# Optimization experiments

Measured on AMD Instinct MI355X. Metric: run time of the kernel, lower is better.

## Reference

```python
import jax, jax.numpy as jnp
import numpy as np

BN_EPS = 1e-5
MIN_DIST = 1e-10

def _three_nn(xyz_up, xyz_down):
    # Pairwise squared distances (B, N, M) via expansion: ||a-b||^2 = |a|^2 + |b|^2 - 2 a.b
    up_sq = jnp.sum(xyz_up * xyz_up, axis=-1, keepdims=True)        # (B, N, 1)
    down_sq = jnp.sum(xyz_down * xyz_down, axis=-1)[:, None, :]      # (B, 1, M)
    cross = jnp.einsum('bnd,bmd->bnm', xyz_up, xyz_down)             # (B, N, M)
    d2 = up_sq + down_sq - 2.0 * cross
    neg_vals, idx = jax.lax.top_k(-d2, 3)                            # 3 smallest dists
    return -neg_vals, idx                                            # (B,N,3), (B,N,3)

def _three_interpolate(features_down, idx, weight):
    # features_down: (B, C, M); idx, weight: (B, N, 3) -> (B, C, N)
    f = jnp.transpose(features_down, (0, 2, 1))                      # (B, M, C)
    gathered = jax.vmap(lambda fm, im: fm[im])(f, idx)               # (B, N, 3, C)
    interp = jnp.einsum('bnkc,bnk->bcn', gathered, weight)           # (B, C, N)
    return interp

def _conv_bn_relu(x, W, gamma, beta):
    # x: (B, C_in, N); W: (C_out, C_in) 1x1 conv, no bias
    y = jnp.einsum('oc,bcn->bon', W, x)
    mean = jnp.mean(y, axis=(0, 2), keepdims=True)
    var = jnp.mean((y - mean) ** 2, axis=(0, 2), keepdims=True)      # biased var (torch BN)
    y = (y - mean) * jax.lax.rsqrt(var + BN_EPS)
    y = y * gamma[None, :, None] + beta[None, :, None]
    return jax.nn.relu(y)

def setup_inputs() -> dict:
    key = jax.random.key(0)
    ks = jax.random.split(key, 8)
    B, N, M = 8, 8192, 2048
    C_down, C_skip = 256, 128
    C_in = C_down + C_skip
    xyz_up = jax.random.normal(ks[0], (B, N, 3), dtype=jnp.float32)
    xyz_down = jax.random.normal(ks[1], (B, M, 3), dtype=jnp.float32)
    features_up = jax.random.normal(ks[2], (B, C_skip, N), dtype=jnp.float32)
    features_down = jax.random.normal(ks[3], (B, C_down, M), dtype=jnp.float32)
    W1 = jax.random.normal(ks[4], (256, C_in), dtype=jnp.float32) * (1.0 / np.sqrt(C_in))
    W2 = jax.random.normal(ks[5], (256, 256), dtype=jnp.float32) * (1.0 / np.sqrt(256))
    g1 = jnp.ones((256,), jnp.float32); b1 = jnp.zeros((256,), jnp.float32)
    g2 = jnp.ones((256,), jnp.float32); b2 = jnp.zeros((256,), jnp.float32)
    return {"xyz_up": xyz_up, "xyz_down": xyz_down, "features_up": features_up,
            "features_down": features_down, "W1": W1, "g1": g1, "b1": b1,
            "W2": W2, "g2": g2, "b2": b2}

def reference(xyz_up, xyz_down, features_up, features_down, W1, g1, b1, W2, g2, b2):
    dist_sq, idx = _three_nn(xyz_up, xyz_down)
    dist_sq = jnp.maximum(dist_sq, MIN_DIST)
    weight = 1.0 / dist_sq
    weight = weight / jnp.sum(weight, axis=-1, keepdims=True)
    interpolated = _three_interpolate(features_down, idx, weight)    # (B, C_down, N)
    combined = jnp.concatenate([interpolated, features_up], axis=1)  # (B, C_in, N)
    h = _conv_bn_relu(combined, W1, g1, b1)
    out = _conv_bn_relu(h, W2, g2, b2)
    return out
```

## Files before the change

kernel.cpp:

```cpp
#include <hip/hip_runtime.h>
#include <hip/hip_bf16.h>

#define NB 8
#define NQ 8192
#define MP 2048
#define CDW 256
#define CSK 128
#define CIN 384
#define COUT 256

typedef __bf16 bf16_t;
typedef bf16_t bf16x8 __attribute__((ext_vector_type(8)));
typedef float f32x4 __attribute__((ext_vector_type(4)));

static __device__ __forceinline__ float bf2f(unsigned short u){
  union { unsigned int ui; float f; } v; v.ui = ((unsigned int)u) << 16; return v.f;
}
static __device__ __forceinline__ unsigned short f2bf(float f){
  union { float f; unsigned int u; } v; v.f = f;
  unsigned int u = v.u;
  return (unsigned short)((u + 0x7FFFu + ((u >> 16) & 1u)) >> 16);
}

__global__ void k_cvt_w(const float* __restrict__ W1, const float* __restrict__ W2,
                        unsigned short* __restrict__ W1b, unsigned short* __restrict__ W2b){
  int i = blockIdx.x * 256 + threadIdx.x;
  if (i < COUT*CIN) W1b[i] = f2bf(W1[i]);
  if (i < COUT*COUT) W2b[i] = f2bf(W2[i]);
}

__global__ __launch_bounds__(256) void k_z(const unsigned short* __restrict__ W1b,
    const float* __restrict__ fd, unsigned short* __restrict__ Z){
  __shared__ unsigned short Bl[64][264];
  int b = blockIdx.y, m0 = blockIdx.x << 6;
  int t = threadIdx.x;
  {
    int m = t & 63, cs0 = t >> 6;
    for (int it = 0; it < 64; ++it){
      int c = cs0 + (it << 2);
      Bl[m][c] = f2bf(fd[((size_t)b*CDW + c)*MP + m0 + m]);
    }
  }
  __syncthreads();
  int l = t & 63, wv = t >> 6;
  int lr = l & 15, lg = l >> 4;
  int ob = wv << 6;
  f32x4 acc[4][4];
  #pragma unroll
  for (int i = 0; i < 4; ++i)
    #pragma unroll
    for (int j = 0; j < 4; ++j)
      acc[i][j] = (f32x4){0.f, 0.f, 0.f, 0.f};
  #pragma unroll 1
  for (int kt = 0; kt < 8; ++kt){
    int k0 = (kt << 5) + (lg << 3);
    bf16x8 af[4], bv[4];
    #pragma unroll
    for (int of = 0; of < 4; ++of)
      af[of] = *(const bf16x8*)(W1b + (size_t)(ob + (of<<4) + lr)*CIN + k0);
    #pragma unroll
    for (int nf = 0; nf < 4; ++nf)
      bv[nf] = *(const bf16x8*)&Bl[(nf<<4) + lr][k0];
    #pragma unroll
    for (int of = 0; of < 4; ++of)
      #pragma unroll
      for (int nf = 0; nf < 4; ++nf)
        acc[of][nf] = __builtin_amdgcn_mfma_f32_16x16x32_bf16(af[of], bv[nf], acc[of][nf], 0, 0, 0);
  }
  #pragma unroll
  for (int of = 0; of < 4; ++of){
    int o = ob + (of<<4) + (lg<<2);
    #pragma unroll
    for (int nf = 0; nf < 4; ++nf){
      int m = m0 + (nf<<4) + lr;
      ushort4 pk;
      pk.x = f2bf(acc[of][nf][0]);
      pk.y = f2bf(acc[of][nf][1]);
      pk.z = f2bf(acc[of][nf][2]);
      pk.w = f2bf(acc[of][nf][3]);
      *(ushort4*)(Z + (((size_t)b*MP + m) << 8) + o) = pk;
    }
  }
}

#define CHUNKS 4
#define MC (MP/CHUNKS)
__global__ __launch_bounds__(256, 2) void k_nn_part(const float* __restrict__ xu, const float* __restrict__ xd,
                                                    float* __restrict__ pd, int* __restrict__ pi){
  int b = blockIdx.z, ch = blockIdx.y, nt = blockIdx.x;
  int t = threadIdx.x;
  __shared__ float4 pts[MC];
  const float* xdb = xd + ((size_t)b*MP + (size_t)ch*MC)*3;
  for (int p = t; p < MC; p += 256){
    float x = xdb[p*3+0], y = xdb[p*3+1], z = xdb[p*3+2];
    pts[p] = make_float4(x, y, z, -0.5f*(x*x + y*y + z*z));
  }
  __syncthreads();
  int n = nt*256 + t;
  const float* q = xu + ((size_t)b*NQ + n)*3;
  float qx = q[0], qy = q[1], qz = q[2];
  float qs = qx*qx + qy*qy + qz*qz;
  float s0 = -3.4e38f, s1 = -3.4e38f, s2 = -3.4e38f;
  int i0 = 0, i1 = 0, i2 = 0;
  #pragma unroll 8
  for (int m = 0; m < MC; ++m){
    float4 p = pts[m];
    float s = fmaf(qz, p.z, fmaf(qy, p.y, fmaf(qx, p.x, p.w)));
    bool c0 = s > s0, c1 = s > s1, c2 = s > s2;
    s2 = c1 ? s1 : (c2 ? s : s2);
    i2 = c1 ? i1 : (c2 ? m : i2);
    s1 = c0 ? s0 : (c1 ? s : s1);
    i1 = c0 ? i0 : (c1 ? m : i1);
    s0 = c0 ? s : s0;
    i0 = c0 ? m : i0;
  }
  int gb = ch*MC;
  size_t base = (((size_t)b*CHUNKS + ch)*NQ + n)*3;
  pd[base+0] = qs - 2.f*s0; pd[base+1] = qs - 2.f*s1; pd[base+2] = qs - 2.f*s2;
  pi[base+0] = gb + i0; pi[base+1] = gb + i1; pi[base+2] = gb + i2;
}

__global__ void k_nn_merge(const float* __restrict__ pd, const int* __restrict__ pi,
                           int* __restrict__ idx3, float* __restrict__ w3){
  int gid = blockIdx.x * 256 + threadIdx.x;
  int b = gid >> 13, n = gid & (NQ-1);
  float d0 = 3.4e38f, d1 = 3.4e38f, d2 = 3.4e38f;
  int i0 = 0, i1 = 0, i2 = 0;
  for (int ch = 0; ch < CHUNKS; ++ch){
    size_t base = (((size_t)b*CHUNKS + ch)*NQ + n)*3;
    #pragma unroll
    for (int k = 0; k < 3; ++k){
      float d = pd[base + k]; int gm = pi[base + k];
      bool c0 = d < d0, c1 = d < d1, c2 = d < d2;
      d2 = c1 ? d1 : (c2 ? d : d2);  i2 = c1 ? i1 : (c2 ? gm : i2);
      d1 = c0 ? d0 : (c1 ? d : d1);  i1 = c0 ? i0 : (c1 ? gm : i1);
      d0 = c0 ? d : d0;              i0 = c0 ? gm : i0;
    }
  }
  float w0 = 1.f / fmaxf(d0, 1e-10f);
  float w1 = 1.f / fmaxf(d1, 1e-10f);
  float w2 = 1.f / fmaxf(d2, 1e-10f);
  float s = w0 + w1 + w2;
  idx3[gid*3+0] = i0; idx3[gid*3+1] = i1; idx3[gid*3+2] = i2;
  w3[gid*3+0] = w0/s; w3[gid*3+1] = w1/s; w3[gid*3+2] = w2/s;
}

__global__ __launch_bounds__(256) void k_fused1(const unsigned short* __restrict__ W1b,
    const float* __restrict__ fu, const int* __restrict__ idx3, const float* __restrict__ w3,
    const unsigned short* __restrict__ Z,
    unsigned short* __restrict__ Y1, float* __restrict__ Sp, float* __restrict__ SSp){
  __shared__ unsigned short Xl[64][136];
  int tile = blockIdx.x;
  int b = tile >> 7;
  int n0 = (tile & 127) << 6;
  int t = threadIdx.x;
  {
    int n = t & 63, cs0 = t >> 6;
    for (int it = 0; it < 32; ++it){
      int cs = cs0 + (it << 2);
      Xl[n][cs] = f2bf(fu[((size_t)b*CSK + cs)*NQ + n0 + n]);
    }
  }
  __syncthreads();
  int l = t & 63, wv = t >> 6;
  int lr = l & 15, lg = l >> 4;
  int ob = wv << 6;
  f32x4 acc[4][4];
  #pragma unroll
  for (int i = 0; i < 4; ++i)
    #pragma unroll
    for (int j = 0; j < 4; ++j)
      acc[i][j] = (f32x4){0.f, 0.f, 0.f, 0.f};
  #pragma unroll 1
  for (int kt = 0; kt < 4; ++kt){
    int k0 = (kt << 5) + (lg << 3);
    bf16x8 af[4], bv[4];
    #pragma unroll
    for (int of = 0; of < 4; ++of)
      af[of] = *(const bf16x8*)(W1b + (size_t)(ob + (of<<4) + lr)*CIN + 256 + k0);
    #pragma unroll
    for (int nf = 0; nf < 4; ++nf)
      bv[nf] = *(const bf16x8*)&Xl[(nf<<4) + lr][k0];
    #pragma unroll
    for (int of = 0; of < 4; ++of)
      #pragma unroll
      for (int nf = 0; nf < 4; ++nf)
        acc[of][nf] = __builtin_amdgcn_mfma_f32_16x16x32_bf16(af[of], bv[nf], acc[of][nf], 0, 0, 0);
  }
  const unsigned short* Zb = Z + (((size_t)b*MP) << 8);
  #pragma unroll
  for (int nf = 0; nf < 4; ++nf){
    int nn = n0 + (nf<<4) + lr;
    int q = ((b << 13) + nn) * 3;
    int j0 = idx3[q], j1 = idx3[q+1], j2 = idx3[q+2];
    float w0 = w3[q], w1 = w3[q+1], w2 = w3[q+2];
    const unsigned short* z0p = Zb + ((size_t)j0 << 8);
    const unsigned short* z1p = Zb + ((size_t)j1 << 8);
    const unsigned short* z2p = Zb + ((size_t)j2 << 8);
    #pragma unroll
    for (int of = 0; of < 4; ++of){
      int o = ob + (of<<4) + (lg<<2);
      ushort4 z0 = *(const ushort4*)(z0p + o);
      ushort4 z1 = *(const ushort4*)(z1p + o);
      ushort4 z2 = *(const ushort4*)(z2p + o);
      acc[of][nf][0] += w0*bf2f(z0.x) + w1*bf2f(z1.x) + w2*bf2f(z2.x);
      acc[of][nf][1] += w0*bf2f(z0.y) + w1*bf2f(z1.y) + w2*bf2f(z2.y);
      acc[of][nf][2] += w0*bf2f(z0.z) + w1*bf2f(z1.z) + w2*bf2f(z2.z);
      acc[of][nf][3] += w0*bf2f(z0.w) + w1*bf2f(z1.w) + w2*bf2f(z2.w);
    }
  }
  #pragma unroll
  for (int of = 0; of < 4; ++of){
    int o = ob + (of<<4) + (lg<<2);
    #pragma unroll
    for (int nf = 0; nf < 4; ++nf){
      int n = n0 + (nf<<4) + lr;
      size_t pos = ((size_t)b << 13) + n;
      ushort4 pk;
      pk.x = f2bf(acc[of][nf][0]);
      pk.y = f2bf(acc[of][nf][1]);
      pk.z = f2bf(acc[of][nf][2]);
      pk.w = f2bf(acc[of][nf][3]);
      *(ushort4*)(Y1 + pos*COUT + o) = pk;
    }
  }
  #pragma unroll
  for (int of = 0; of < 4; ++of){
    #pragma unroll
    for (int r = 0; r < 4; ++r){
      float sv = acc[of][0][r] + acc[of][1][r] + acc[of][2][r] + acc[of][3][r];
      float sq = acc[of][0][r]*acc[of][0][r] + acc[of][1][r]*acc[of][1][r]
               + acc[of][2][r]*acc[of][2][r] + acc[of][3][r]*acc[of][3][r];
      #pragma unroll
      for (int off = 1; off < 16; off <<= 1){
        sv += __shfl_xor(sv, off);
        sq += __shfl_xor(sq, off);
      }
      if (lr == 0){
        int o = ob + (of<<4) + (lg<<2) + r;
        Sp[(size_t)tile*256 + o] = sv;
        SSp[(size_t)tile*256 + o] = sq;
      }
    }
  }
}

__global__ __launch_bounds__(256) void k_reduce(const float* __restrict__ Sp, const float* __restrict__ SSp,
                                                float* __restrict__ Sr, float* __restrict__ SSr){
  int t = threadIdx.x;
  int w = blockIdx.x * 4 + (t >> 6);
  int lane = t & 63;
  const float* src = (w < 256) ? Sp : SSp;
  int o = w & 255;
  float s = 0.f;
  #pragma unroll
  for (int j = 0; j < 16; ++j)
    s += src[(size_t)(lane + (j << 6))*256 + o];
  #pragma unroll
  for (int off = 1; off < 64; off <<= 1) s += __shfl_xor(s, off);
  if (lane == 0){
    if (w < 256) Sr[o] = s; else SSr[o] = s;
  }
}

__global__ void k_finalize(const float* __restrict__ S, const float* __restrict__ SS,
                           const float* __restrict__ g, const float* __restrict__ be,
                           float* __restrict__ scale, float* __restrict__ shift){
  int o = threadIdx.x;
  const float cnt = 65536.f;
  float mean = S[o] / cnt;
  float var = SS[o] / cnt - mean*mean;
  float inv = rsqrtf(var + 1e-5f);
  float sc = g[o] * inv;
  scale[o] = sc;
  shift[o] = be[o] - mean * sc;
}

__global__ __launch_bounds__(256) void k_gemm2(const unsigned short* __restrict__ W2b,
    const unsigned short* __restrict__ Y1, const float* __restrict__ scale1,
    const float* __restrict__ shift1, unsigned short* __restrict__ Y2,
    float* __restrict__ Sp, float* __restrict__ SSp){
  __shared__ unsigned short buf[256*68];
  int tile = blockIdx.x;
  int b = tile >> 7;
  int n0 = (tile & 127) << 6;
  int t = threadIdx.x;
  {
    int nn0 = t >> 6;
    int cb = (t & 63) << 2;
    float scl[4], shl[4];
    #pragma unroll
    for (int j = 0; j < 4; ++j){ scl[j] = scale1[cb+j]; shl[j] = shift1[cb+j]; }
    for (int it = 0; it < 16; ++it){
      int nn = nn0 + (it << 2);
      size_t pos = ((size_t)b << 13) + n0 + nn;
      ushort4 a = *(const ushort4*)(Y1 + pos*COUT + cb);
      ushort4 r;
      r.x = f2bf(fmaxf(bf2f(a.x)*scl[0] + shl[0], 0.f));
      r.y = f2bf(fmaxf(bf2f(a.y)*scl[1] + shl[1], 0.f));
      r.z = f2bf(fmaxf(bf2f(a.z)*scl[2] + shl[2], 0.f));
      r.w = f2bf(fmaxf(bf2f(a.w)*scl[3] + shl[3], 0.f));
      *(ushort4*)&buf[nn*264 + cb] = r;
    }
  }
  __syncthreads();
  int l = t & 63, wv = t >> 6;
  int lr = l & 15, lg = l >> 4;
  int ob = wv << 6;
  f32x4 acc[4][4];
  #pragma unroll
  for (int i = 0; i < 4; ++i)
    #pragma unroll
    for (int j = 0; j < 4; ++j)
      acc[i][j] = (f32x4){0.f, 0.f, 0.f, 0.f};
  #pragma unroll 1
  for (int kt = 0; kt < 8; ++kt){
    int k0 = (kt << 5) + (lg << 3);
    bf16x8 af[4], bv[4];
    #pragma unroll
    for (int of = 0; of < 4; ++of)
      af[of] = *(const bf16x8*)(W2b + (size_t)(ob + (of<<4) + lr)*COUT + k0);
    #pragma unroll
    for (int nf = 0; nf < 4; ++nf)
      bv[nf] = *(const bf16x8*)&buf[((nf<<4) + lr)*264 + k0];
    #pragma unroll
    for (int of = 0; of < 4; ++of)
      #pragma unroll
      for (int nf = 0; nf < 4; ++nf)
        acc[of][nf] = __builtin_amdgcn_mfma_f32_16x16x32_bf16(af[of], bv[nf], acc[of][nf], 0, 0, 0);
  }
  #pragma unroll
  for (int of = 0; of < 4; ++of){
    #pragma unroll
    for (int r = 0; r < 4; ++r){
      float sv = acc[of][0][r] + acc[of][1][r] + acc[of][2][r] + acc[of][3][r];
      float sq = acc[of][0][r]*acc[of][0][r] + acc[of][1][r]*acc[of][1][r]
               + acc[of][2][r]*acc[of][2][r] + acc[of][3][r]*acc[of][3][r];
      #pragma unroll
      for (int off = 1; off < 16; off <<= 1){
        sv += __shfl_xor(sv, off);
        sq += __shfl_xor(sq, off);
      }
      if (lr == 0){
        int o = ob + (of<<4) + (lg<<2) + r;
        Sp[(size_t)tile*256 + o] = sv;
        SSp[(size_t)tile*256 + o] = sq;
      }
    }
  }
  __syncthreads();
  #pragma unroll
  for (int of = 0; of < 4; ++of){
    int o = ob + (of<<4) + (lg<<2);
    #pragma unroll
    for (int nf = 0; nf < 4; ++nf){
      int n = (nf<<4) + lr;
      #pragma unroll
      for (int r = 0; r < 4; ++r)
        buf[(o + r)*68 + n] = f2bf(acc[of][nf][r]);
    }
  }
  __syncthreads();
  {
    int nx = (t & 31) << 1;
    int og = t >> 5;
    for (int it = 0; it < 32; ++it){
      int o = og + (it << 3);
      unsigned int v = (unsigned int)buf[o*68 + nx] | ((unsigned int)buf[o*68 + nx + 1] << 16);
      *(unsigned int*)(Y2 + (((size_t)b*COUT + o) << 13) + n0 + nx) = v;
    }
  }
}

__global__ void k_out(const unsigned short* __restrict__ Y2,
                      const float* __restrict__ scale2, const float* __restrict__ shift2,
                      float* __restrict__ out){
  size_t i = (size_t)blockIdx.x * 256 + threadIdx.x;
  size_t e = i << 2;
  int o = (int)((e >> 13) & 255);
  ushort4 v = *(const ushort4*)(Y2 + e);
  float sc = scale2[o], sh = shift2[o];
  float4 r;
  r.x = fmaxf(bf2f(v.x)*sc + sh, 0.f);
  r.y = fmaxf(bf2f(v.y)*sc + sh, 0.f);
  r.z = fmaxf(bf2f(v.z)*sc + sh, 0.f);
  r.w = fmaxf(bf2f(v.w)*sc + sh, 0.f);
  *(float4*)(out + e) = r;
}

extern "C" void kernel_launch(void* const* d_in, const int* in_sizes, int n_in,
                              void* d_out, int out_size, void* d_ws, size_t ws_size,
                              hipStream_t stream) {
  (void)in_sizes; (void)n_in; (void)out_size; (void)ws_size;
  const float* xu = (const float*)d_in[0];
  const float* xd = (const float*)d_in[1];
  const float* fu = (const float*)d_in[2];
  const float* fd = (const float*)d_in[3];
  const float* W1 = (const float*)d_in[4];
  const float* g1 = (const float*)d_in[5];
  const float* b1 = (const float*)d_in[6];
  const float* W2 = (const float*)d_in[7];
  const float* g2 = (const float*)d_in[8];
  const float* b2 = (const float*)d_in[9];
  float* out = (float*)d_out;

  char* w = (char*)d_ws;
  size_t off = 0;
  unsigned short* Z   = (unsigned short*)(w + off); off += (size_t)NB*MP*256*2;
  unsigned short* W1b = (unsigned short*)(w + off); off += (size_t)COUT*CIN*2;
  unsigned short* W2b = (unsigned short*)(w + off); off += (size_t)COUT*COUT*2;
  float* pd  = (float*)(w + off); off += (size_t)NB*CHUNKS*NQ*3*4;
  int*   pi  = (int*)(w + off);   off += (size_t)NB*CHUNKS*NQ*3*4;
  int*   idx3= (int*)(w + off);   off += (size_t)NB*NQ*3*4;
  float* w3  = (float*)(w + off); off += (size_t)NB*NQ*3*4;
  unsigned short* Y1 = (unsigned short*)(w + off); off += (size_t)NB*NQ*COUT*2;
  unsigned short* Y2 = (unsigned short*)(w + off); off += (size_t)NB*NQ*COUT*2;
  float* Sp1  = (float*)(w + off); off += (size_t)1024*256*4;
  float* SSp1 = (float*)(w + off); off += (size_t)1024*256*4;
  float* Sp2  = (float*)(w + off); off += (size_t)1024*256*4;
  float* SSp2 = (float*)(w + off); off += (size_t)1024*256*4;
  float* Sr1  = (float*)(w + off); off += 256*4;
  float* SSr1 = (float*)(w + off); off += 256*4;
  float* Sr2  = (float*)(w + off); off += 256*4;
  float* SSr2 = (float*)(w + off); off += 256*4;
  float* scale1 = (float*)(w + off); off += 256*4;
  float* shift1 = (float*)(w + off); off += 256*4;
  float* scale2 = (float*)(w + off); off += 256*4;
  float* shift2 = (float*)(w + off); off += 256*4;

  k_cvt_w<<<dim3(384), dim3(256), 0, stream>>>(W1, W2, W1b, W2b);
  k_z<<<dim3(32, 8), dim3(256), 0, stream>>>(W1b, fd, Z);
  k_nn_part<<<dim3(32, 4, 8), dim3(256), 0, stream>>>(xu, xd, pd, pi);
  k_nn_merge<<<dim3(256), dim3(256), 0, stream>>>(pd, pi, idx3, w3);
  k_fused1<<<dim3(1024), dim3(256), 0, stream>>>(W1b, fu, idx3, w3, Z, Y1, Sp1, SSp1);
  k_reduce<<<dim3(128), dim3(256), 0, stream>>>(Sp1, SSp1, Sr1, SSr1);
  k_finalize<<<dim3(1), dim3(256), 0, stream>>>(Sr1, SSr1, g1, b1, scale1, shift1);
  k_gemm2<<<dim3(1024), dim3(256), 0, stream>>>(W2b, Y1, scale1, shift1, Y2, Sp2, SSp2);
  k_reduce<<<dim3(128), dim3(256), 0, stream>>>(Sp2, SSp2, Sr2, SSr2);
  k_finalize<<<dim3(1), dim3(256), 0, stream>>>(Sr2, SSr2, g2, b2, scale2, shift2);
  k_out<<<dim3(16384), dim3(256), 0, stream>>>(Y2, scale2, shift2, out);
}
```

Before: 189.8 us.

## Process two queries per thread with inline-asm top-3 in NN search

The nearest-neighbour partial kernel now has each thread track two query points, so every shared-memory point load is reused for two distance evaluations. The top-3 insertion is written as hand-scheduled v_fma/v_cmp/v_cndmask inline assembly, interleaved across the two queries for more instruction-level parallelism. To keep the block count the same, the point set is split into 8 chunks instead of 4. In exchange, the merge kernel reads twice as many partial candidates, and the pd/pi workspace must be sized for 8 chunks.

```diff
diff --git a/kernel.cpp b/kernel.cpp
--- a/kernel.cpp
+++ b/kernel.cpp
@@ -83,41 +83,93 @@
   }
 }
 
-#define CHUNKS 4
+#define CHUNKS 8
 #define MC (MP/CHUNKS)
+
+#define NN_STEP2(P)                                                          \
+  asm("v_fma_f32 %[sa], %[qxa], %[px], %[pw]\n\t"                            \
+      "v_fma_f32 %[sb], %[qxb], %[px], %[pw]\n\t"                            \
+      "v_fma_f32 %[sa], %[qya], %[py], %[sa]\n\t"                            \
+      "v_fma_f32 %[sb], %[qyb], %[py], %[sb]\n\t"                            \
+      "v_fma_f32 %[sa], %[qza], %[pz], %[sa]\n\t"                            \
+      "v_fma_f32 %[sb], %[qzb], %[pz], %[sb]\n\t"                            \
+      "v_cmp_gt_f32 %[m1a], %[sa], %[s1a]\n\t"                               \
+      "v_cmp_gt_f32 %[m1b], %[sb], %[s1b]\n\t"                               \
+      "v_cmp_gt_f32 %[m2a], %[sa], %[s2a]\n\t"                               \
+      "v_cmp_gt_f32 %[m2b], %[sb], %[s2b]\n\t"                               \
+      "v_cndmask_b32 %[s2a], %[s2a], %[sa], %[m2a]\n\t"                      \
+      "v_cndmask_b32 %[s2b], %[s2b], %[sb], %[m2b]\n\t"                      \
+      "v_cndmask_b32 %[i2a], %[i2a], %[mi], %[m2a]\n\t"                      \
+      "v_cndmask_b32 %[i2b], %[i2b], %[mi], %[m2b]\n\t"                      \
+      "v_cndmask_b32 %[s2a], %[s2a], %[s1a], %[m1a]\n\t"                     \
+      "v_cndmask_b32 %[s2b], %[s2b], %[s1b], %[m1b]\n\t"                     \
+      "v_cndmask_b32 %[i2a], %[i2a], %[i1a], %[m1a]\n\t"                     \
+      "v_cndmask_b32 %[i2b], %[i2b], %[i1b], %[m1b]\n\t"                     \
+      "v_cmp_gt_f32 %[m2a], %[sa], %[s0a]\n\t"                               \
+      "v_cmp_gt_f32 %[m2b], %[sb], %[s0b]\n\t"                               \
+      "v_cndmask_b32 %[s1a], %[s1a], %[sa], %[m1a]\n\t"                      \
+      "v_cndmask_b32 %[s1b], %[s1b], %[sb], %[m1b]\n\t"                      \
+      "v_cndmask_b32 %[i1a], %[i1a], %[mi], %[m1a]\n\t"                      \
+      "v_cndmask_b32 %[i1b], %[i1b], %[mi], %[m1b]\n\t"                      \
+      "v_cndmask_b32 %[s1a], %[s1a], %[s0a], %[m2a]\n\t"                     \
+      "v_cndmask_b32 %[s1b], %[s1b], %[s0b], %[m2b]\n\t"                     \
+      "v_cndmask_b32 %[i1a], %[i1a], %[i0a], %[m2a]\n\t"                     \
+      "v_cndmask_b32 %[i1b], %[i1b], %[i0b], %[m2b]\n\t"                     \
+      "v_cndmask_b32 %[s0a], %[s0a], %[sa], %[m2a]\n\t"                      \
+      "v_cndmask_b32 %[s0b], %[s0b], %[sb], %[m2b]\n\t"                      \
+      "v_cndmask_b32 %[i0a], %[i0a], %[mi], %[m2a]\n\t"                      \
+      "v_cndmask_b32 %[i0b], %[i0b], %[mi], %[m2b]\n\t"                      \
+      "v_add_u32 %[mi], 1, %[mi]\n\t"                                        \
+      : [sa]"=&v"(sva), [sb]"=&v"(svb),                                      \
+        [m1a]"=&s"(mk1a), [m2a]"=&s"(mk2a), [m1b]"=&s"(mk1b), [m2b]"=&s"(mk2b),\
+        [s0a]"+v"(s0a), [s1a]"+v"(s1a), [s2a]"+v"(s2a),                      \
+        [i0a]"+v"(i0a), [i1a]"+v"(i1a), [i2a]"+v"(i2a),                      \
+        [s0b]"+v"(s0b), [s1b]"+v"(s1b), [s2b]"+v"(s2b),                      \
+        [i0b]"+v"(i0b), [i1b]"+v"(i1b), [i2b]"+v"(i2b), [mi]"+v"(mi)         \
+      : [qxa]"v"(qxa), [qya]"v"(qya), [qza]"v"(qza),                         \
+        [qxb]"v"(qxb), [qyb]"v"(qyb), [qzb]"v"(qzb),                         \
+        [px]"v"((P).x), [py]"v"((P).y), [pz]"v"((P).z), [pw]"v"((P).w))
+
 __global__ __launch_bounds__(256, 2) void k_nn_part(const float* __restrict__ xu, const float* __restrict__ xd,
                                                     float* __restrict__ pd, int* __restrict__ pi){
   int b = blockIdx.z, ch = blockIdx.y, nt = blockIdx.x;
   int t = threadIdx.x;
   __shared__ float4 pts[MC];
   const float* xdb = xd + ((size_t)b*MP + (size_t)ch*MC)*3;
-  for (int p = t; p < MC; p += 256){
+  if (t < MC){
+    int p = t;
     float x = xdb[p*3+0], y = xdb[p*3+1], z = xdb[p*3+2];
     pts[p] = make_float4(x, y, z, -0.5f*(x*x + y*y + z*z));
   }
   __syncthreads();
-  int n = nt*256 + t;
-  const float* q = xu + ((size_t)b*NQ + n)*3;
-  float qx = q[0], qy = q[1], qz = q[2];
-  float qs = qx*qx + qy*qy + qz*qz;
-  float s0 = -3.4e38f, s1 = -3.4e38f, s2 = -3.4e38f;
-  int i0 = 0, i1 = 0, i2 = 0;
-  #pragma unroll 8
-  for (int m = 0; m < MC; ++m){
-    float4 p = pts[m];
-    float s = fmaf(qz, p.z, fmaf(qy, p.y, fmaf(qx, p.x, p.w)));
-    bool c0 = s > s0, c1 = s > s1, c2 = s > s2;
-    s2 = c1 ? s1 : (c2 ? s : s2);
-    i2 = c1 ? i1 : (c2 ? m : i2);
-    s1 = c0 ? s0 : (c1 ? s : s1);
-    i1 = c0 ? i0 : (c1 ? m : i1);
-    s0 = c0 ? s : s0;
-    i0 = c0 ? m : i0;
+  int na = nt*512 + t;
+  int nb_ = na + 256;
+  const float* qa = xu + ((size_t)b*NQ + na)*3;
+  const float* qb = xu + ((size_t)b*NQ + nb_)*3;
+  float qxa = qa[0], qya = qa[1], qza = qa[2];
+  float qxb = qb[0], qyb = qb[1], qzb = qb[2];
+  float qsa = qxa*qxa + qya*qya + qza*qza;
+  float qsb = qxb*qxb + qyb*qyb + qzb*qzb;
+  float s0a = -3.4e38f, s1a = -3.4e38f, s2a = -3.4e38f;
+  float s0b = -3.4e38f, s1b = -3.4e38f, s2b = -3.4e38f;
+  int i0a = 0, i1a = 0, i2a = 0, i0b = 0, i1b = 0, i2b = 0;
+  int mi = 0;
+  float sva, svb;
+  unsigned long long mk1a, mk2a, mk1b, mk2b;
+  #pragma unroll 1
+  for (int mb = 0; mb < MC; mb += 8){
+    float4 P0 = pts[mb+0], P1 = pts[mb+1], P2 = pts[mb+2], P3 = pts[mb+3];
+    float4 P4 = pts[mb+4], P5 = pts[mb+5], P6 = pts[mb+6], P7 = pts[mb+7];
+    NN_STEP2(P0); NN_STEP2(P1); NN_STEP2(P2); NN_STEP2(P3);
+    NN_STEP2(P4); NN_STEP2(P5); NN_STEP2(P6); NN_STEP2(P7);
   }
   int gb = ch*MC;
-  size_t base = (((size_t)b*CHUNKS + ch)*NQ + n)*3;
-  pd[base+0] = qs - 2.f*s0; pd[base+1] = qs - 2.f*s1; pd[base+2] = qs - 2.f*s2;
-  pi[base+0] = gb + i0; pi[base+1] = gb + i1; pi[base+2] = gb + i2;
+  size_t basea = (((size_t)b*CHUNKS + ch)*NQ + na)*3;
+  pd[basea+0] = qsa - 2.f*s0a; pd[basea+1] = qsa - 2.f*s1a; pd[basea+2] = qsa - 2.f*s2a;
+  pi[basea+0] = gb + i0a; pi[basea+1] = gb + i1a; pi[basea+2] = gb + i2a;
+  size_t baseb = (((size_t)b*CHUNKS + ch)*NQ + nb_)*3;
+  pd[baseb+0] = qsb - 2.f*s0b; pd[baseb+1] = qsb - 2.f*s1b; pd[baseb+2] = qsb - 2.f*s2b;
+  pi[baseb+0] = gb + i0b; pi[baseb+1] = gb + i1b; pi[baseb+2] = gb + i2b;
 }
 
 __global__ void k_nn_merge(const float* __restrict__ pd, const int* __restrict__ pi,
@@ -430,7 +482,7 @@
 
   k_cvt_w<<<dim3(384), dim3(256), 0, stream>>>(W1, W2, W1b, W2b);
   k_z<<<dim3(32, 8), dim3(256), 0, stream>>>(W1b, fd, Z);
-  k_nn_part<<<dim3(32, 4, 8), dim3(256), 0, stream>>>(xu, xd, pd, pi);
+  k_nn_part<<<dim3(16, 8, 8), dim3(256), 0, stream>>>(xu, xd, pd, pi);
   k_nn_merge<<<dim3(256), dim3(256), 0, stream>>>(pd, pi, idx3, w3);
   k_fused1<<<dim3(1024), dim3(256), 0, stream>>>(W1b, fu, idx3, w3, Z, Y1, Sp1, SSp1);
   k_reduce<<<dim3(128), dim3(256), 0, stream>>>(Sp1, SSp1, Sr1, SSr1);
```

Result: no change. 188.3 us (-0.8%).

## Rewrite three-NN with scalar-operand inline asm and fuse BN reduce/finalize

Applied to the files above, without the earlier changes.

Database points are packed as float4 (coordinates plus -0.5 squared norm) once in the weight-convert kernel. The chunked NN search plus merge kernel is replaced by a single kernel that scans all M points per query. It loads the points through uniform, scalar-friendly global reads and runs hand-written inline asm that uses SGPR point operands and SGPR compare masks with cndmask top-3 updates. The two BN stat reduce and finalize kernels are merged into one per layer, removing two launches and the intermediate buffers. The tradeoff is less parallelism in the NN kernel (256 blocks instead of 1024) and reliance on the compiler placing the point data in SGPRs.

```diff
diff --git a/kernel.cpp b/kernel.cpp
--- a/kernel.cpp
+++ b/kernel.cpp
@@ -23,10 +23,16 @@
 }
 
 __global__ void k_cvt_w(const float* __restrict__ W1, const float* __restrict__ W2,
-                        unsigned short* __restrict__ W1b, unsigned short* __restrict__ W2b){
+                        const float* __restrict__ xd,
+                        unsigned short* __restrict__ W1b, unsigned short* __restrict__ W2b,
+                        float4* __restrict__ pts4){
   int i = blockIdx.x * 256 + threadIdx.x;
   if (i < COUT*CIN) W1b[i] = f2bf(W1[i]);
   if (i < COUT*COUT) W2b[i] = f2bf(W2[i]);
+  if (i < NB*MP){
+    float x = xd[i*3+0], y = xd[i*3+1], z = xd[i*3+2];
+    pts4[i] = make_float4(x, y, z, -0.5f*(x*x + y*y + z*z));
+  }
 }
 
 __global__ __launch_bounds__(256) void k_z(const unsigned short* __restrict__ W1b,
@@ -83,66 +89,60 @@
   }
 }
 
-#define CHUNKS 4
-#define MC (MP/CHUNKS)
-__global__ __launch_bounds__(256, 2) void k_nn_part(const float* __restrict__ xu, const float* __restrict__ xd,
-                                                    float* __restrict__ pd, int* __restrict__ pi){
-  int b = blockIdx.z, ch = blockIdx.y, nt = blockIdx.x;
-  int t = threadIdx.x;
-  __shared__ float4 pts[MC];
-  const float* xdb = xd + ((size_t)b*MP + (size_t)ch*MC)*3;
-  for (int p = t; p < MC; p += 256){
-    float x = xdb[p*3+0], y = xdb[p*3+1], z = xdb[p*3+2];
-    pts[p] = make_float4(x, y, z, -0.5f*(x*x + y*y + z*z));
-  }
-  __syncthreads();
-  int n = nt*256 + t;
+#define NN_S(P)                                                              \
+  asm("v_mul_f32 %[s], %[px], %[qx]\n\t"                                     \
+      "v_fma_f32 %[s], %[py], %[qy], %[s]\n\t"                               \
+      "v_fma_f32 %[s], %[pz], %[qz], %[s]\n\t"                               \
+      "v_add_f32 %[s], %[pw], %[s]\n\t"                                      \
+      "v_cmp_gt_f32 %[m2], %[s], %[s2]\n\t"                                  \
+      "v_cmp_gt_f32 %[m1], %[s], %[s1]\n\t"                                  \
+      "v_cmp_gt_f32 %[m0], %[s], %[s0]\n\t"                                  \
+      "v_cndmask_b32 %[s2], %[s2], %[s], %[m2]\n\t"                          \
+      "v_cndmask_b32 %[i2], %[i2], %[mi], %[m2]\n\t"                         \
+      "v_cndmask_b32 %[s2], %[s2], %[s1], %[m1]\n\t"                         \
+      "v_cndmask_b32 %[i2], %[i2], %[i1], %[m1]\n\t"                         \
+      "v_cndmask_b32 %[s1], %[s1], %[s], %[m1]\n\t"                          \
+      "v_cndmask_b32 %[i1], %[i1], %[mi], %[m1]\n\t"                         \
+      "v_cndmask_b32 %[s1], %[s1], %[s0], %[m0]\n\t"                         \
+      "v_cndmask_b32 %[i1], %[i1], %[i0], %[m0]\n\t"                         \
+      "v_cndmask_b32 %[s0], %[s0], %[s], %[m0]\n\t"                          \
+      "v_cndmask_b32 %[i0], %[i0], %[mi], %[m0]\n\t"                         \
+      "v_add_u32 %[mi], 1, %[mi]\n\t"                                        \
+      : [s]"=&v"(sv),                                                        \
+        [m0]"=&s"(mk0), [m1]"=&s"(mk1), [m2]"=&s"(mk2),                      \
+        [s0]"+v"(s0), [s1]"+v"(s1), [s2]"+v"(s2),                            \
+        [i0]"+v"(i0), [i1]"+v"(i1), [i2]"+v"(i2), [mi]"+v"(mi)               \
+      : [qx]"v"(qx), [qy]"v"(qy), [qz]"v"(qz),                               \
+        [px]"s"((P).x), [py]"s"((P).y), [pz]"s"((P).z), [pw]"s"((P).w))
+
+__global__ __launch_bounds__(256) void k_nn(const float* __restrict__ xu,
+                                            const float4* __restrict__ pts4,
+                                            int* __restrict__ idx3, float* __restrict__ w3){
+  int b = blockIdx.y;
+  int n = blockIdx.x * 256 + threadIdx.x;
+  const float4* pts = pts4 + (size_t)b * MP;
   const float* q = xu + ((size_t)b*NQ + n)*3;
   float qx = q[0], qy = q[1], qz = q[2];
   float qs = qx*qx + qy*qy + qz*qz;
   float s0 = -3.4e38f, s1 = -3.4e38f, s2 = -3.4e38f;
-  int i0 = 0, i1 = 0, i2 = 0;
-  #pragma unroll 8
-  for (int m = 0; m < MC; ++m){
-    float4 p = pts[m];
-    float s = fmaf(qz, p.z, fmaf(qy, p.y, fmaf(qx, p.x, p.w)));
-    bool c0 = s > s0, c1 = s > s1, c2 = s > s2;
-    s2 = c1 ? s1 : (c2 ? s : s2);
-    i2 = c1 ? i1 : (c2 ? m : i2);
-    s1 = c0 ? s0 : (c1 ? s : s1);
-    i1 = c0 ? i0 : (c1 ? m : i1);
-    s0 = c0 ? s : s0;
-    i0 = c0 ? m : i0;
-  }
-  int gb = ch*MC;
-  size_t base = (((size_t)b*CHUNKS + ch)*NQ + n)*3;
-  pd[base+0] = qs - 2.f*s0; pd[base+1] = qs - 2.f*s1; pd[base+2] = qs - 2.f*s2;
-  pi[base+0] = gb + i0; pi[base+1] = gb + i1; pi[base+2] = gb + i2;
-}
-
-__global__ void k_nn_merge(const float* __restrict__ pd, const int* __restrict__ pi,
-                           int* __restrict__ idx3, float* __restrict__ w3){
-  int gid = blockIdx.x * 256 + threadIdx.x;
-  int b = gid >> 13, n = gid & (NQ-1);
-  float d0 = 3.4e38f, d1 = 3.4e38f, d2 = 3.4e38f;
-  int i0 = 0, i1 = 0, i2 = 0;
-  for (int ch = 0; ch < CHUNKS; ++ch){
-    size_t base = (((size_t)b*CHUNKS + ch)*NQ + n)*3;
-    #pragma unroll
-    for (int k = 0; k < 3; ++k){
-      float d = pd[base + k]; int gm = pi[base + k];
-      bool c0 = d < d0, c1 = d < d1, c2 = d < d2;
-      d2 = c1 ? d1 : (c2 ? d : d2);  i2 = c1 ? i1 : (c2 ? gm : i2);
-      d1 = c0 ? d0 : (c1 ? d : d1);  i1 = c0 ? i0 : (c1 ? gm : i1);
-      d0 = c0 ? d : d0;              i0 = c0 ? gm : i0;
-    }
-  }
-  float w0 = 1.f / fmaxf(d0, 1e-10f);
-  float w1 = 1.f / fmaxf(d1, 1e-10f);
-  float w2 = 1.f / fmaxf(d2, 1e-10f);
-  float s = w0 + w1 + w2;
+  int i0 = 0, i1 = 0, i2 = 0, mi = 0;
+  float sv;
+  unsigned long long mk0, mk1, mk2;
+  #pragma unroll 1
+  for (int mb = 0; mb < MP; mb += 8){
+    float4 P0 = pts[mb+0], P1 = pts[mb+1], P2 = pts[mb+2], P3 = pts[mb+3];
+    float4 P4 = pts[mb+4], P5 = pts[mb+5], P6 = pts[mb+6], P7 = pts[mb+7];
+    NN_S(P0); NN_S(P1); NN_S(P2); NN_S(P3);
+    NN_S(P4); NN_S(P5); NN_S(P6); NN_S(P7);
+  }
+  float d0 = fmaxf(qs - 2.f*s0, 1e-10f);
+  float d1 = fmaxf(qs - 2.f*s1, 1e-10f);
+  float d2 = fmaxf(qs - 2.f*s2, 1e-10f);
+  float w0 = 1.f/d0, w1 = 1.f/d1, w2 = 1.f/d2;
+  float ssum = w0 + w1 + w2;
+  int gid = (b << 13) + n;
   idx3[gid*3+0] = i0; idx3[gid*3+1] = i1; idx3[gid*3+2] = i2;
-  w3[gid*3+0] = w0/s; w3[gid*3+1] = w1/s; w3[gid*3+2] = w2/s;
+  w3[gid*3+0] = w0/ssum; w3[gid*3+1] = w1/ssum; w3[gid*3+2] = w2/ssum;
 }
 
 __global__ __launch_bounds__(256) void k_fused1(const unsigned short* __restrict__ W1b,
@@ -245,35 +245,30 @@
   }
 }
 
-__global__ __launch_bounds__(256) void k_reduce(const float* __restrict__ Sp, const float* __restrict__ SSp,
-                                                float* __restrict__ Sr, float* __restrict__ SSr){
+__global__ __launch_bounds__(256) void k_reduce2(const float* __restrict__ Sp, const float* __restrict__ SSp,
+    const float* __restrict__ g, const float* __restrict__ be,
+    float* __restrict__ scale, float* __restrict__ shift){
   int t = threadIdx.x;
-  int w = blockIdx.x * 4 + (t >> 6);
+  int o = blockIdx.x * 4 + (t >> 6);
   int lane = t & 63;
-  const float* src = (w < 256) ? Sp : SSp;
-  int o = w & 255;
-  float s = 0.f;
-  #pragma unroll
-  for (int j = 0; j < 16; ++j)
-    s += src[(size_t)(lane + (j << 6))*256 + o];
-  #pragma unroll
-  for (int off = 1; off < 64; off <<= 1) s += __shfl_xor(s, off);
+  float s = 0.f, ss = 0.f;
+  #pragma unroll
+  for (int j = 0; j < 16; ++j){
+    size_t row = (size_t)(lane + (j << 6))*256 + o;
+    s += Sp[row]; ss += SSp[row];
+  }
+  #pragma unroll
+  for (int off = 1; off < 64; off <<= 1){
+    s += __shfl_xor(s, off); ss += __shfl_xor(ss, off);
+  }
   if (lane == 0){
-    if (w < 256) Sr[o] = s; else SSr[o] = s;
-  }
-}
-
-__global__ void k_finalize(const float* __restrict__ S, const float* __restrict__ SS,
-                           const float* __restrict__ g, const float* __restrict__ be,
-                           float* __restrict__ scale, float* __restrict__ shift){
-  int o = threadIdx.x;
-  const float cnt = 65536.f;
-  float mean = S[o] / cnt;
-  float var = SS[o] / cnt - mean*mean;
-  float inv = rsqrtf(var + 1e-5f);
-  float sc = g[o] * inv;
-  scale[o] = sc;
-  shift[o] = be[o] - mean * sc;
+    float mean = s / 65536.f;
+    float var = ss / 65536.f - mean*mean;
+    float inv = rsqrtf(var + 1e-5f);
+    float sc = g[o] * inv;
+    scale[o] = sc;
+    shift[o] = be[o] - mean * sc;
+  }
 }
 
 __global__ __launch_bounds__(256) void k_gemm2(const unsigned short* __restrict__ W2b,
@@ -409,8 +404,7 @@
   unsigned short* Z   = (unsigned short*)(w + off); off += (size_t)NB*MP*256*2;
   unsigned short* W1b = (unsigned short*)(w + off); off += (size_t)COUT*CIN*2;
   unsigned short* W2b = (unsigned short*)(w + off); off += (size_t)COUT*COUT*2;
-  float* pd  = (float*)(w + off); off += (size_t)NB*CHUNKS*NQ*3*4;
-  int*   pi  = (int*)(w + off);   off += (size_t)NB*CHUNKS*NQ*3*4;
+  float4* pts4 = (float4*)(w + off); off += (size_t)NB*MP*16;
   int*   idx3= (int*)(w + off);   off += (size_t)NB*NQ*3*4;
   float* w3  = (float*)(w + off); off += (size_t)NB*NQ*3*4;
   unsigned short* Y1 = (unsigned short*)(w + off); off += (size_t)NB*NQ*COUT*2;
@@ -419,24 +413,17 @@
   float* SSp1 = (float*)(w + off); off += (size_t)1024*256*4;
   float* Sp2  = (float*)(w + off); off += (size_t)1024*256*4;
   float* SSp2 = (float*)(w + off); off += (size_t)1024*256*4;
-  float* Sr1  = (float*)(w + off); off += 256*4;
-  float* SSr1 = (float*)(w + off); off += 256*4;
-  float* Sr2  = (float*)(w + off); off += 256*4;
-  float* SSr2 = (float*)(w + off); off += 256*4;
   float* scale1 = (float*)(w + off); off += 256*4;
   float* shift1 = (float*)(w + off); off += 256*4;
   float* scale2 = (float*)(w + off); off += 256*4;
   float* shift2 = (float*)(w + off); off += 256*4;
 
-  k_cvt_w<<<dim3(384), dim3(256), 0, stream>>>(W1, W2, W1b, W2b);
+  k_cvt_w<<<dim3(384), dim3(256), 0, stream>>>(W1, W2, xd, W1b, W2b, pts4);
   k_z<<<dim3(32, 8), dim3(256), 0, stream>>>(W1b, fd, Z);
-  k_nn_part<<<dim3(32, 4, 8), dim3(256), 0, stream>>>(xu, xd, pd, pi);
-  k_nn_merge<<<dim3(256), dim3(256), 0, stream>>>(pd, pi, idx3, w3);
+  k_nn<<<dim3(32, 8), dim3(256), 0, stream>>>(xu, pts4, idx3, w3);
   k_fused1<<<dim3(1024), dim3(256), 0, stream>>>(W1b, fu, idx3, w3, Z, Y1, Sp1, SSp1);
-  k_reduce<<<dim3(128), dim3(256), 0, stream>>>(Sp1, SSp1, Sr1, SSr1);
-  k_finalize<<<dim3(1), dim3(256), 0, stream>>>(Sr1, SSr1, g1, b1, scale1, shift1);
+  k_reduce2<<<dim3(64), dim3(256), 0, stream>>>(Sp1, SSp1, g1, b1, scale1, shift1);
   k_gemm2<<<dim3(1024), dim3(256), 0, stream>>>(W2b, Y1, scale1, shift1, Y2, Sp2, SSp2);
-  k_reduce<<<dim3(128), dim3(256), 0, stream>>>(Sp2, SSp2, Sr2, SSr2);
-  k_finalize<<<dim3(1), dim3(256), 0, stream>>>(Sr2, SSr2, g2, b2, scale2, shift2);
+  k_reduce2<<<dim3(64), dim3(256), 0, stream>>>(Sp2, SSp2, g2, b2, scale2, shift2);
   k_out<<<dim3(16384), dim3(256), 0, stream>>>(Y2, scale2, shift2, out);
 }
```

Result: slower. 277.6 us (+46.3%).
